# Kernel optimization log

Measured on AMD Instinct MI355X. Metric: run time of the kernel, lower is better.

Reference implementation:

```python
import jax, jax.numpy as jnp
import numpy as np
from jax import lax


def ternary_quantize(w):
    # alpha = mean(|w|); threshold = 0.7*alpha; map to {-1,0,1}*alpha
    alpha = jnp.mean(jnp.abs(w))
    threshold = 0.7 * alpha
    w_ternary = jnp.where(jnp.abs(w) < threshold, jnp.zeros_like(w), jnp.sign(w))
    return alpha * w_ternary


def setup_inputs() -> dict:
    key = jax.random.key(0)
    k1, k2 = jax.random.split(key)
    B, L, Cin = 32, 8192, 1
    K, F = 16, 256
    x = jax.random.normal(k1, (B, L, Cin), dtype=jnp.float32)
    # matches keras RandomUniform(-0.1, 0.1) initializer
    w = jax.random.uniform(k2, (K, Cin, F), dtype=jnp.float32, minval=-0.1, maxval=0.1)
    b = jnp.zeros((F,), dtype=jnp.float32)
    return {"x": x, "w": w, "b": b}


def reference(x, w, b):
    # x: (B, L, Cin) NWC; w: (K, Cin, F) WIO; stride 1, padding SAME
    w_q = ternary_quantize(w)
    y = lax.conv_general_dilated(
        x, w_q,
        window_strides=(1,),
        padding="SAME",
        dimension_numbers=("NWC", "WIO", "NWC"),
    )
    return y + b
```

## Files before the change

### kernel.cpp

```cpp
#include <hip/hip_runtime.h>
#include <hip/hip_bf16.h>

typedef float f32x4 __attribute__((ext_vector_type(4)));

__global__ __launch_bounds__(256) void ternary_conv1d_fused(
    const float* __restrict__ x,
    const float* __restrict__ w,
    const float* __restrict__ bias,
    float* __restrict__ y,
    int L) {
    const int t  = threadIdx.x;
    const int fg = t & 63;
    const int ls = t >> 6;
    const int bid = blockIdx.x;
    const int b  = bid >> 5;
    const int g  = bid & 31;
    const int lbase = g * 256;

    __shared__ float red[256];
    __shared__ float xs[80];
    __shared__ float alpha_s;

    float s = 0.f;
#pragma unroll
    for (int j = 0; j < 16; ++j) s += fabsf(w[t + 256 * j]);
    red[t] = s;
    __syncthreads();
    for (int off = 128; off > 0; off >>= 1) {
        if (t < off) red[t] += red[t + off];
        __syncthreads();
    }
    if (t == 0) alpha_s = red[0] * (1.0f / 4096.0f);
    __syncthreads();
    const float alpha = alpha_s;
    const float thr = 0.7f * alpha;

    f32x4 wv[16];
#pragma unroll
    for (int k = 0; k < 16; ++k) {
        f32x4 v = *reinterpret_cast<const f32x4*>(w + k * 256 + fg * 4);
        f32x4 q;
#pragma unroll
        for (int c = 0; c < 4; ++c) {
            float vc = v[c];
            float tc = (fabsf(vc) < thr) ? 0.f : (vc > 0.f ? 1.f : (vc < 0.f ? -1.f : 0.f));
            q[c] = alpha * tc;
        }
        wv[k] = q;
    }
    const f32x4 bv = *reinterpret_cast<const f32x4*>(bias + fg * 4);

    for (int tt = 0; tt < 4; ++tt) {
        const int l0 = lbase + tt * 64;
        __syncthreads();
        if (t < 79) {
            int gl = l0 - 7 + t;
            xs[t] = (gl >= 0 && gl < L) ? x[(size_t)b * L + gl] : 0.f;
        }
        __syncthreads();

        float xw[16];
#pragma unroll
        for (int j = 0; j < 16; ++j) xw[j] = xs[ls + j];

        f32x4* outp = reinterpret_cast<f32x4*>(y) + ((size_t)b * L + l0 + ls) * 64 + fg;
#pragma unroll
        for (int i = 0; i < 16; ++i) {
            f32x4 acc = bv;
#pragma unroll
            for (int k = 0; k < 16; ++k) {
                acc += wv[k] * xw[k];
            }
            *outp = acc;
            outp += 256;
            if (i < 15) {
#pragma unroll
                for (int j = 0; j < 12; ++j) xw[j] = xw[j + 4];
#pragma unroll
                for (int j = 12; j < 16; ++j) xw[j] = xs[ls + 4 * (i + 1) + j];
            }
        }
    }
}

extern "C" void kernel_launch(void* const* d_in, const int* in_sizes, int n_in,
                              void* d_out, int out_size, void* d_ws, size_t ws_size,
                              hipStream_t stream) {
    const float* x = (const float*)d_in[0];
    const float* w = (const float*)d_in[1];
    const float* b = (const float*)d_in[2];
    float* y = (float*)d_out;

    const int B = 32;
    const int L = in_sizes[0] / B;

    ternary_conv1d_fused<<<B * 32, 256, 0, stream>>>(x, w, b, y, L);
}
```

Measured before the change: 51.63 us.

## Compute alpha with wave shuffles and halve per-block length tile

Replaces the shared-memory tree reduction for alpha with per-thread sums over the weights already loaded, followed by a 64-lane shuffle reduction. Each wave covers all 4096 weights, so every wave gets the full sum without block barriers or a second pass over w. The block's 128-sample x window is loaded once up front, before the weight work, removing the per-subtile barriers. The grid doubles to 2048 blocks of 128 positions each, which gives more parallelism but repeats the weight quantization per block.

```diff
diff --git a/kernel.cpp b/kernel.cpp
--- a/kernel.cpp
+++ b/kernel.cpp
@@ -13,72 +13,64 @@
     const int fg = t & 63;
     const int ls = t >> 6;
     const int bid = blockIdx.x;
-    const int b  = bid >> 5;
-    const int g  = bid & 31;
-    const int lbase = g * 256;
+    const int b  = bid >> 6;
+    const int g  = bid & 63;
+    const int lbase = g * 128;
 
-    __shared__ float red[256];
-    __shared__ float xs[80];
-    __shared__ float alpha_s;
+    __shared__ float xs[144];
 
-    float s = 0.f;
-#pragma unroll
-    for (int j = 0; j < 16; ++j) s += fabsf(w[t + 256 * j]);
-    red[t] = s;
-    __syncthreads();
-    for (int off = 128; off > 0; off >>= 1) {
-        if (t < off) red[t] += red[t + off];
-        __syncthreads();
+    if (t < 143) {
+        int gl = lbase - 7 + t;
+        xs[t] = (gl >= 0 && gl < L) ? x[(size_t)b * L + gl] : 0.f;
     }
-    if (t == 0) alpha_s = red[0] * (1.0f / 4096.0f);
-    __syncthreads();
-    const float alpha = alpha_s;
-    const float thr = 0.7f * alpha;
 
     f32x4 wv[16];
+    float s = 0.f;
 #pragma unroll
     for (int k = 0; k < 16; ++k) {
         f32x4 v = *reinterpret_cast<const f32x4*>(w + k * 256 + fg * 4);
-        f32x4 q;
+        wv[k] = v;
+        s += fabsf(v.x) + fabsf(v.y) + fabsf(v.z) + fabsf(v.w);
+    }
+#pragma unroll
+    for (int m = 1; m < 64; m <<= 1) s += __shfl_xor(s, m, 64);
+    const float alpha = s * (1.0f / 4096.0f);
+    const float thr = 0.7f * alpha;
+
+#pragma unroll
+    for (int k = 0; k < 16; ++k) {
+        f32x4 v = wv[k], q;
 #pragma unroll
         for (int c = 0; c < 4; ++c) {
             float vc = v[c];
-            float tc = (fabsf(vc) < thr) ? 0.f : (vc > 0.f ? 1.f : (vc < 0.f ? -1.f : 0.f));
-            q[c] = alpha * tc;
+            q[c] = (fabsf(vc) < thr) ? 0.f
+                 : (vc > 0.f ? alpha : (vc < 0.f ? -alpha : 0.f));
         }
         wv[k] = q;
     }
     const f32x4 bv = *reinterpret_cast<const f32x4*>(bias + fg * 4);
 
-    for (int tt = 0; tt < 4; ++tt) {
-        const int l0 = lbase + tt * 64;
-        __syncthreads();
-        if (t < 79) {
-            int gl = l0 - 7 + t;
-            xs[t] = (gl >= 0 && gl < L) ? x[(size_t)b * L + gl] : 0.f;
+    __syncthreads();
+
+    float xw[16];
+#pragma unroll
+    for (int j = 0; j < 16; ++j) xw[j] = xs[ls + j];
+
+    f32x4* outp = reinterpret_cast<f32x4*>(y) + ((size_t)b * L + lbase + ls) * 64 + fg;
+#pragma unroll
+    for (int i = 0; i < 32; ++i) {
+        f32x4 acc = bv;
+#pragma unroll
+        for (int k = 0; k < 16; ++k) {
+            acc += wv[k] * xw[k];
         }
-        __syncthreads();
-
-        float xw[16];
+        *outp = acc;
+        outp += 256;
+        if (i < 31) {
 #pragma unroll
-        for (int j = 0; j < 16; ++j) xw[j] = xs[ls + j];
-
-        f32x4* outp = reinterpret_cast<f32x4*>(y) + ((size_t)b * L + l0 + ls) * 64 + fg;
+            for (int j = 0; j < 12; ++j) xw[j] = xw[j + 4];
 #pragma unroll
-        for (int i = 0; i < 16; ++i) {
-            f32x4 acc = bv;
-#pragma unroll
-            for (int k = 0; k < 16; ++k) {
-                acc += wv[k] * xw[k];
-            }
-            *outp = acc;
-            outp += 256;
-            if (i < 15) {
-#pragma unroll
-                for (int j = 0; j < 12; ++j) xw[j] = xw[j + 4];
-#pragma unroll
-                for (int j = 12; j < 16; ++j) xw[j] = xs[ls + 4 * (i + 1) + j];
-            }
+            for (int j = 12; j < 16; ++j) xw[j] = xs[ls + 4 * (i + 1) + j];
         }
     }
 }
@@ -94,5 +86,5 @@
     const int B = 32;
     const int L = in_sizes[0] / B;
 
-    ternary_conv1d_fused<<<B * 32, 256, 0, stream>>>(x, w, b, y, L);
+    ternary_conv1d_fused<<<B * 64, 256, 0, stream>>>(x, w, b, y, L);
 }
```

Measured after the change: 52.03 us. No clear change (+0.8%).
